# Kernel optimization log

Hardware: AMD Instinct MI355X
Metric: run time of the kernel (lower is better)

The kernel has to match this reference:

```python
import jax, jax.numpy as jnp
import numpy as np
import math

D = 512      # input_size == hidden_size
TAU = 4      # length of att/spatial lists
N = 16384    # tokens (batch*H*W)

def setup_inputs() -> dict:
    key = jax.random.key(0)
    ks = jax.random.split(key, 16)
    s = 1.0 / math.sqrt(D)
    return {
        "T_t": jax.random.normal(ks[0], (N, D), jnp.float32),
        "S_t": jax.random.normal(ks[1], (N, D), jnp.float32),
        "t_att": jax.random.normal(ks[2], (TAU, N, D), jnp.float32),
        "s_att": jax.random.normal(ks[3], (TAU, N, D), jnp.float32),
        "t_spatial": jax.random.normal(ks[4], (TAU, N, D), jnp.float32),
        "s_spatial": jax.random.normal(ks[5], (TAU, N, D), jnp.float32),
        # fl_t: Linear(D, 3D); fl_t_next: Linear(D, D); same for s
        "W_t": jax.random.uniform(ks[6], (3 * D, D), jnp.float32, -s, s),
        "b_t": jax.random.uniform(ks[7], (3 * D,), jnp.float32, -s, s),
        "W_tn": jax.random.uniform(ks[8], (D, D), jnp.float32, -s, s),
        "b_tn": jax.random.uniform(ks[9], (D,), jnp.float32, -s, s),
        "W_s": jax.random.uniform(ks[10], (3 * D, D), jnp.float32, -s, s),
        "b_s": jax.random.uniform(ks[11], (3 * D,), jnp.float32, -s, s),
        "W_sn": jax.random.uniform(ks[12], (D, D), jnp.float32, -s, s),
        "b_sn": jax.random.uniform(ks[13], (D,), jnp.float32, -s, s),
    }

def reference(T_t, S_t, t_att, s_att, t_spatial, s_spatial,
              W_t, b_t, W_tn, b_tn, W_s, b_s, W_sn, b_sn):
    d = T_t.shape[-1]
    scale = 1.0 / jnp.sqrt(jnp.asarray(d, T_t.dtype))
    s_next = S_t @ W_sn.T + b_sn          # [N, D]
    t_next = T_t @ W_tn.T + b_tn          # [N, D]

    # trend weights: dot-product along feature dim, softmax over tau axis
    w_s = jax.nn.softmax(jnp.einsum('knd,nd->kn', s_att, s_next) * scale, axis=0)
    w_t = jax.nn.softmax(jnp.einsum('knd,nd->kn', t_spatial, t_next) * scale, axis=0)
    T_trend = jnp.einsum('knd,kn->nd', t_att, w_s)      # [N, D]
    S_trend = jnp.einsum('knd,kn->nd', s_spatial, w_t)  # [N, D]

    t_gate = jax.nn.sigmoid(t_next)
    s_gate = jax.nn.sigmoid(s_next)
    T_fusion = T_t * t_gate + (1.0 - t_gate) * T_trend
    S_fusion = S_t * s_gate + (1.0 - s_gate) * S_trend

    T_concat = T_fusion @ W_t.T + b_t     # [N, 3D]
    S_concat = S_fusion @ W_s.T + b_s
    t_g, t_t, t_s = jnp.split(T_concat, 3, axis=1)
    s_g, s_t, s_s = jnp.split(S_concat, 3, axis=1)
    T_gate = jax.nn.sigmoid(t_g)
    S_gate = jax.nn.sigmoid(s_g)
    T_new = T_gate * t_t + (1.0 - T_gate) * s_t
    S_new = S_gate * s_s + (1.0 - S_gate) * t_s
    return T_new, S_new
```

## Files before the change

kernel.cpp:

```cpp
#include <hip/hip_runtime.h>

#define NTOK 16384
#define DIM 512
#define NTAU 4

typedef __attribute__((ext_vector_type(4))) float f32x4;
typedef __attribute__((ext_vector_type(8))) short bf16x8;
typedef __attribute__((ext_vector_type(4))) unsigned short u16x4;
typedef __attribute__((ext_vector_type(8))) unsigned short u16x8;

__device__ inline unsigned short f2bf(float f) {
    union { float f; unsigned int u; } v; v.f = f;
    unsigned int u = v.u + 0x7FFFu + ((v.u >> 16) & 1u);
    return (unsigned short)(u >> 16);
}

__global__ void convert_f32_bf16(const float* __restrict__ src,
                                 unsigned short* __restrict__ dst, int n4) {
    int i = blockIdx.x * blockDim.x + threadIdx.x;
    if (i < n4) {
        f32x4 v = ((const f32x4*)src)[i];
        u16x4 o;
        o[0] = f2bf(v[0]); o[1] = f2bf(v[1]); o[2] = f2bf(v[2]); o[3] = f2bf(v[3]);
        ((u16x4*)dst)[i] = o;
    }
}

__global__ __launch_bounds__(256, 2) void gemm_next(
    const float* __restrict__ A, const unsigned short* __restrict__ W,
    const float* __restrict__ bias, float* __restrict__ out)
{
    __shared__ unsigned short lA[128][40];
    __shared__ unsigned short lB[128][40];
    const int tid = threadIdx.x;
    const int m0 = blockIdx.y * 128;
    const int n0 = blockIdx.x * 128;
    const int lane = tid & 63;
    const int w = tid >> 6;
    const int wr = w >> 1, wc = w & 1;

    f32x4 acc[4][4];
#pragma unroll
    for (int i = 0; i < 4; i++)
#pragma unroll
        for (int j = 0; j < 4; j++) acc[i][j] = (f32x4){0.f, 0.f, 0.f, 0.f};

    const int arow = tid >> 3;
    const int acol = (tid & 7) * 4;
    const int brow = tid >> 2;
    const int bcol = (tid & 3) * 8;

    for (int k0 = 0; k0 < DIM; k0 += 32) {
#pragma unroll
        for (int i = 0; i < 4; i++) {
            int r = arow + 32 * i;
            f32x4 v = *(const f32x4*)(A + (size_t)(m0 + r) * DIM + k0 + acol);
            u16x4 o;
            o[0] = f2bf(v[0]); o[1] = f2bf(v[1]); o[2] = f2bf(v[2]); o[3] = f2bf(v[3]);
            *(u16x4*)&lA[r][acol] = o;
        }
#pragma unroll
        for (int i = 0; i < 2; i++) {
            int r = brow + 64 * i;
            u16x8 v = *(const u16x8*)(W + (size_t)(n0 + r) * DIM + k0 + bcol);
            *(u16x8*)&lB[r][bcol] = v;
        }
        __syncthreads();

        bf16x8 af[4], bfr[4];
#pragma unroll
        for (int i = 0; i < 4; i++)
            af[i] = *(const bf16x8*)&lA[wr * 64 + i * 16 + (lane & 15)][(lane >> 4) * 8];
#pragma unroll
        for (int j = 0; j < 4; j++)
            bfr[j] = *(const bf16x8*)&lB[wc * 64 + j * 16 + (lane & 15)][(lane >> 4) * 8];
#pragma unroll
        for (int i = 0; i < 4; i++)
#pragma unroll
            for (int j = 0; j < 4; j++)
                acc[i][j] = __builtin_amdgcn_mfma_f32_16x16x32_bf16(af[i], bfr[j], acc[i][j], 0, 0, 0);
        __syncthreads();
    }

#pragma unroll
    for (int j = 0; j < 4; j++) {
        int n = n0 + wc * 64 + j * 16 + (lane & 15);
        float bv = bias[n];
#pragma unroll
        for (int i = 0; i < 4; i++) {
            int mbase = m0 + wr * 64 + i * 16 + (lane >> 4) * 4;
#pragma unroll
            for (int r = 0; r < 4; r++)
                out[(size_t)(mbase + r) * DIM + n] = acc[i][j][r] + bv;
        }
    }
}

__global__ __launch_bounds__(256) void fuse_stream(
    const float* __restrict__ T_t, const float* __restrict__ S_t,
    const float* __restrict__ t_att, const float* __restrict__ s_att,
    const float* __restrict__ t_spatial, const float* __restrict__ s_spatial,
    const float* __restrict__ t_next, const float* __restrict__ s_next,
    unsigned short* __restrict__ Tf, unsigned short* __restrict__ Sf)
{
    const int lane = threadIdx.x & 63;
    const int wave = blockIdx.x * (blockDim.x >> 6) + (threadIdx.x >> 6);
    const int nwaves = gridDim.x * (blockDim.x >> 6);
    const float scale = 0.04419417382415922f;

    for (int n = wave; n < NTOK; n += nwaves) {
        const size_t rb = (size_t)n * DIM;
        const int c0 = lane * 4, c1 = 256 + lane * 4;
        f32x4 tn_a = *(const f32x4*)(t_next + rb + c0);
        f32x4 tn_b = *(const f32x4*)(t_next + rb + c1);
        f32x4 sn_a = *(const f32x4*)(s_next + rb + c0);
        f32x4 sn_b = *(const f32x4*)(s_next + rb + c1);

        float dws[NTAU], dwt[NTAU];
#pragma unroll
        for (int k = 0; k < NTAU; k++) {
            const size_t kb = ((size_t)k * NTOK + n) * DIM;
            f32x4 sa = *(const f32x4*)(s_att + kb + c0);
            f32x4 sb = *(const f32x4*)(s_att + kb + c1);
            f32x4 ta = *(const f32x4*)(t_spatial + kb + c0);
            f32x4 tb = *(const f32x4*)(t_spatial + kb + c1);
            dws[k] = sa[0]*sn_a[0]+sa[1]*sn_a[1]+sa[2]*sn_a[2]+sa[3]*sn_a[3]
                   + sb[0]*sn_b[0]+sb[1]*sn_b[1]+sb[2]*sn_b[2]+sb[3]*sn_b[3];
            dwt[k] = ta[0]*tn_a[0]+ta[1]*tn_a[1]+ta[2]*tn_a[2]+ta[3]*tn_a[3]
                   + tb[0]*tn_b[0]+tb[1]*tn_b[1]+tb[2]*tn_b[2]+tb[3]*tn_b[3];
        }
#pragma unroll
        for (int k = 0; k < NTAU; k++) {
            float v = dws[k];
#pragma unroll
            for (int off = 32; off; off >>= 1) v += __shfl_xor(v, off);
            dws[k] = v * scale;
            float u = dwt[k];
#pragma unroll
            for (int off = 32; off; off >>= 1) u += __shfl_xor(u, off);
            dwt[k] = u * scale;
        }
        float ms = fmaxf(fmaxf(dws[0], dws[1]), fmaxf(dws[2], dws[3]));
        float mt = fmaxf(fmaxf(dwt[0], dwt[1]), fmaxf(dwt[2], dwt[3]));
        float ws_[NTAU], wt_[NTAU], ssum = 0.f, tsum = 0.f;
#pragma unroll
        for (int k = 0; k < NTAU; k++) {
            ws_[k] = __expf(dws[k] - ms); ssum += ws_[k];
            wt_[k] = __expf(dwt[k] - mt); tsum += wt_[k];
        }
        float rs = 1.f / ssum, rt = 1.f / tsum;
#pragma unroll
        for (int k = 0; k < NTAU; k++) { ws_[k] *= rs; wt_[k] *= rt; }

        f32x4 Tta = {0,0,0,0}, Ttb = {0,0,0,0}, Sta = {0,0,0,0}, Stb = {0,0,0,0};
#pragma unroll
        for (int k = 0; k < NTAU; k++) {
            const size_t kb = ((size_t)k * NTOK + n) * DIM;
            f32x4 ta = *(const f32x4*)(t_att + kb + c0);
            f32x4 tb = *(const f32x4*)(t_att + kb + c1);
            f32x4 sa = *(const f32x4*)(s_spatial + kb + c0);
            f32x4 sb = *(const f32x4*)(s_spatial + kb + c1);
            float wk = ws_[k], vk = wt_[k];
#pragma unroll
            for (int e = 0; e < 4; e++) {
                Tta[e] += wk * ta[e]; Ttb[e] += wk * tb[e];
                Sta[e] += vk * sa[e]; Stb[e] += vk * sb[e];
            }
        }
        f32x4 Ta = *(const f32x4*)(T_t + rb + c0);
        f32x4 Tb = *(const f32x4*)(T_t + rb + c1);
        f32x4 Sa = *(const f32x4*)(S_t + rb + c0);
        f32x4 Sb = *(const f32x4*)(S_t + rb + c1);

        u16x4 oTa, oTb, oSa, oSb;
#pragma unroll
        for (int e = 0; e < 4; e++) {
            float gt_a = 1.f / (1.f + __expf(-tn_a[e]));
            float gt_b = 1.f / (1.f + __expf(-tn_b[e]));
            float gs_a = 1.f / (1.f + __expf(-sn_a[e]));
            float gs_b = 1.f / (1.f + __expf(-sn_b[e]));
            oTa[e] = f2bf(Ta[e] * gt_a + (1.f - gt_a) * Tta[e]);
            oTb[e] = f2bf(Tb[e] * gt_b + (1.f - gt_b) * Ttb[e]);
            oSa[e] = f2bf(Sa[e] * gs_a + (1.f - gs_a) * Sta[e]);
            oSb[e] = f2bf(Sb[e] * gs_b + (1.f - gs_b) * Stb[e]);
        }
        *(u16x4*)(Tf + rb + c0) = oTa;
        *(u16x4*)(Tf + rb + c1) = oTb;
        *(u16x4*)(Sf + rb + c0) = oSa;
        *(u16x4*)(Sf + rb + c1) = oSb;
    }
}

__global__ __launch_bounds__(256, 2) void gemm_final(
    const unsigned short* __restrict__ Tf, const unsigned short* __restrict__ Sf,
    const unsigned short* __restrict__ Wt, const unsigned short* __restrict__ Ws,
    const float* __restrict__ bt, const float* __restrict__ bs,
    float* __restrict__ out)
{
    __shared__ unsigned short lT[128][40];
    __shared__ unsigned short lS[128][40];
    __shared__ unsigned short lW[6][32][40];
    const int tid = threadIdx.x;
    const int m0 = blockIdx.y * 128;
    const int j0 = blockIdx.x * 32;
    const int lane = tid & 63;
    const int w = tid >> 6, wr = w >> 1, wc = w & 1;

    f32x4 acc[6][4];
#pragma unroll
    for (int g = 0; g < 6; g++)
#pragma unroll
        for (int i = 0; i < 4; i++) acc[g][i] = (f32x4){0.f, 0.f, 0.f, 0.f};

    const int arow = tid >> 2;
    const int acol = (tid & 3) * 8;

    for (int k0 = 0; k0 < DIM; k0 += 32) {
#pragma unroll
        for (int i = 0; i < 2; i++) {
            int r = arow + 64 * i;
            *(u16x8*)&lT[r][acol] = *(const u16x8*)(Tf + (size_t)(m0 + r) * DIM + k0 + acol);
            *(u16x8*)&lS[r][acol] = *(const u16x8*)(Sf + (size_t)(m0 + r) * DIM + k0 + acol);
        }
#pragma unroll
        for (int i = 0; i < 3; i++) {
            int c = tid + 256 * i;
            int g = c >> 7;
            int rr = (c >> 2) & 31;
            int ch = (c & 3) * 8;
            const unsigned short* src = (g < 3) ? Wt : Ws;
            int row = (g % 3) * DIM + j0 + rr;
            *(u16x8*)&lW[g][rr][ch] = *(const u16x8*)(src + (size_t)row * DIM + k0 + ch);
        }
        __syncthreads();

        bf16x8 aT[4], aS[4];
#pragma unroll
        for (int i = 0; i < 4; i++) {
            aT[i] = *(const bf16x8*)&lT[wr * 64 + i * 16 + (lane & 15)][(lane >> 4) * 8];
            aS[i] = *(const bf16x8*)&lS[wr * 64 + i * 16 + (lane & 15)][(lane >> 4) * 8];
        }
#pragma unroll
        for (int g = 0; g < 6; g++) {
            bf16x8 bw = *(const bf16x8*)&lW[g][wc * 16 + (lane & 15)][(lane >> 4) * 8];
#pragma unroll
            for (int i = 0; i < 4; i++)
                acc[g][i] = __builtin_amdgcn_mfma_f32_16x16x32_bf16(
                    (g < 3) ? aT[i] : aS[i], bw, acc[g][i], 0, 0, 0);
        }
        __syncthreads();
    }

    const int j = j0 + wc * 16 + (lane & 15);
    const float btg = bt[j], btt = bt[512 + j], bts = bt[1024 + j];
    const float bsg = bs[j], bst = bs[512 + j], bss = bs[1024 + j];
#pragma unroll
    for (int i = 0; i < 4; i++) {
        int mbase = m0 + wr * 64 + i * 16 + (lane >> 4) * 4;
#pragma unroll
        for (int r = 0; r < 4; r++) {
            float TG = acc[0][i][r] + btg;
            float TT = acc[1][i][r] + btt;
            float TS = acc[2][i][r] + bts;
            float SG = acc[3][i][r] + bsg;
            float ST = acc[4][i][r] + bst;
            float SS = acc[5][i][r] + bss;
            float gT = 1.f / (1.f + __expf(-TG));
            float gS = 1.f / (1.f + __expf(-SG));
            size_t m = (size_t)(mbase + r);
            out[m * DIM + j] = gT * TT + (1.f - gT) * ST;
            out[(size_t)NTOK * DIM + m * DIM + j] = gS * SS + (1.f - gS) * TS;
        }
    }
}

extern "C" void kernel_launch(void* const* d_in, const int* in_sizes, int n_in,
                              void* d_out, int out_size, void* d_ws, size_t ws_size,
                              hipStream_t stream) {
    const float* T_t       = (const float*)d_in[0];
    const float* S_t       = (const float*)d_in[1];
    const float* t_att     = (const float*)d_in[2];
    const float* s_att     = (const float*)d_in[3];
    const float* t_spatial = (const float*)d_in[4];
    const float* s_spatial = (const float*)d_in[5];
    const float* W_t  = (const float*)d_in[6];
    const float* b_t  = (const float*)d_in[7];
    const float* W_tn = (const float*)d_in[8];
    const float* b_tn = (const float*)d_in[9];
    const float* W_s  = (const float*)d_in[10];
    const float* b_s  = (const float*)d_in[11];
    const float* W_sn = (const float*)d_in[12];
    const float* b_sn = (const float*)d_in[13];
    float* out = (float*)d_out;

    char* ws = (char*)d_ws;
    float*          t_next = (float*)(ws + 0);
    float*          s_next = (float*)(ws + 33554432);
    unsigned short* Tf     = (unsigned short*)(ws + 67108864);
    unsigned short* Sf     = (unsigned short*)(ws + 83886080);
    unsigned short* Wtn_b  = (unsigned short*)(ws + 100663296);
    unsigned short* Wsn_b  = (unsigned short*)(ws + 101187584);
    unsigned short* Wt_b   = (unsigned short*)(ws + 101711872);
    unsigned short* Ws_b   = (unsigned short*)(ws + 103284736);

    const int n_sq = 512 * 512 / 4, n_big = 1536 * 512 / 4;
    convert_f32_bf16<<<(n_sq + 255) / 256, 256, 0, stream>>>(W_tn, Wtn_b, n_sq);
    convert_f32_bf16<<<(n_sq + 255) / 256, 256, 0, stream>>>(W_sn, Wsn_b, n_sq);
    convert_f32_bf16<<<(n_big + 255) / 256, 256, 0, stream>>>(W_t, Wt_b, n_big);
    convert_f32_bf16<<<(n_big + 255) / 256, 256, 0, stream>>>(W_s, Ws_b, n_big);

    dim3 g1(DIM / 128, NTOK / 128);
    gemm_next<<<g1, 256, 0, stream>>>(T_t, Wtn_b, b_tn, t_next);
    gemm_next<<<g1, 256, 0, stream>>>(S_t, Wsn_b, b_sn, s_next);

    fuse_stream<<<2048, 256, 0, stream>>>(T_t, S_t, t_att, s_att, t_spatial, s_spatial,
                                          t_next, s_next, Tf, Sf);

    dim3 g3(DIM / 32, NTOK / 128);
    gemm_final<<<g3, 256, 0, stream>>>(Tf, Sf, Wt_b, Ws_b, b_t, b_s, out);
}
```

Baseline: 303.0 us.

## Store next-projections as bf16 and process two tokens per wave with nontemporal loads

The t_next/s_next intermediates are now written by gemm_next as bf16 instead of fp32, which halves their write and read traffic between kernels. fuse_stream drops the grid-stride loop: each wave handles two tokens, each lane covers 8 contiguous features, and the streamed att/spatial tensors are read with nontemporal loads. The goal is less memory traffic and more loads in flight in this bandwidth-bound stage. The cost is lower precision in the gate and softmax-logit inputs, which now pass through bf16.

Result: no change. 305.8 us (+0.9%).

```diff
diff --git a/kernel.cpp b/kernel.cpp
--- a/kernel.cpp
+++ b/kernel.cpp
@@ -14,6 +14,16 @@
     unsigned int u = v.u + 0x7FFFu + ((v.u >> 16) & 1u);
     return (unsigned short)(u >> 16);
 }
+
+__device__ inline void bf8_to_f32(u16x8 h, f32x4& a, f32x4& b) {
+    union { unsigned int u; float f; } t;
+#pragma unroll
+    for (int e = 0; e < 4; e++) { t.u = ((unsigned int)h[e]) << 16; a[e] = t.f; }
+#pragma unroll
+    for (int e = 0; e < 4; e++) { t.u = ((unsigned int)h[4 + e]) << 16; b[e] = t.f; }
+}
+
+#define NTLOAD4(p) __builtin_nontemporal_load((const f32x4*)(p))
 
 __global__ void convert_f32_bf16(const float* __restrict__ src,
                                  unsigned short* __restrict__ dst, int n4) {
@@ -28,7 +38,7 @@
 
 __global__ __launch_bounds__(256, 2) void gemm_next(
     const float* __restrict__ A, const unsigned short* __restrict__ W,
-    const float* __restrict__ bias, float* __restrict__ out)
+    const float* __restrict__ bias, unsigned short* __restrict__ out)
 {
     __shared__ unsigned short lA[128][40];
     __shared__ unsigned short lB[128][40];
@@ -91,7 +101,7 @@
             int mbase = m0 + wr * 64 + i * 16 + (lane >> 4) * 4;
 #pragma unroll
             for (int r = 0; r < 4; r++)
-                out[(size_t)(mbase + r) * DIM + n] = acc[i][j][r] + bv;
+                out[(size_t)(mbase + r) * DIM + n] = f2bf(acc[i][j][r] + bv);
         }
     }
 }
@@ -100,94 +110,106 @@
     const float* __restrict__ T_t, const float* __restrict__ S_t,
     const float* __restrict__ t_att, const float* __restrict__ s_att,
     const float* __restrict__ t_spatial, const float* __restrict__ s_spatial,
-    const float* __restrict__ t_next, const float* __restrict__ s_next,
+    const unsigned short* __restrict__ t_next, const unsigned short* __restrict__ s_next,
     unsigned short* __restrict__ Tf, unsigned short* __restrict__ Sf)
 {
     const int lane = threadIdx.x & 63;
-    const int wave = blockIdx.x * (blockDim.x >> 6) + (threadIdx.x >> 6);
-    const int nwaves = gridDim.x * (blockDim.x >> 6);
+    const int w = blockIdx.x * 4 + (threadIdx.x >> 6);
     const float scale = 0.04419417382415922f;
-
-    for (int n = wave; n < NTOK; n += nwaves) {
-        const size_t rb = (size_t)n * DIM;
-        const int c0 = lane * 4, c1 = 256 + lane * 4;
-        f32x4 tn_a = *(const f32x4*)(t_next + rb + c0);
-        f32x4 tn_b = *(const f32x4*)(t_next + rb + c1);
-        f32x4 sn_a = *(const f32x4*)(s_next + rb + c0);
-        f32x4 sn_b = *(const f32x4*)(s_next + rb + c1);
-
-        float dws[NTAU], dwt[NTAU];
+    const int c = lane * 8;
+
+    const int n[2] = { 2 * w, 2 * w + 1 };
+    f32x4 tn_a[2], tn_b[2], sn_a[2], sn_b[2];
+#pragma unroll
+    for (int t = 0; t < 2; t++) {
+        const size_t rb = (size_t)n[t] * DIM + c;
+        bf8_to_f32(*(const u16x8*)(t_next + rb), tn_a[t], tn_b[t]);
+        bf8_to_f32(*(const u16x8*)(s_next + rb), sn_a[t], sn_b[t]);
+    }
+
+    float dws[2][NTAU], dwt[2][NTAU];
+#pragma unroll
+    for (int t = 0; t < 2; t++) {
 #pragma unroll
         for (int k = 0; k < NTAU; k++) {
-            const size_t kb = ((size_t)k * NTOK + n) * DIM;
-            f32x4 sa = *(const f32x4*)(s_att + kb + c0);
-            f32x4 sb = *(const f32x4*)(s_att + kb + c1);
-            f32x4 ta = *(const f32x4*)(t_spatial + kb + c0);
-            f32x4 tb = *(const f32x4*)(t_spatial + kb + c1);
-            dws[k] = sa[0]*sn_a[0]+sa[1]*sn_a[1]+sa[2]*sn_a[2]+sa[3]*sn_a[3]
-                   + sb[0]*sn_b[0]+sb[1]*sn_b[1]+sb[2]*sn_b[2]+sb[3]*sn_b[3];
-            dwt[k] = ta[0]*tn_a[0]+ta[1]*tn_a[1]+ta[2]*tn_a[2]+ta[3]*tn_a[3]
-                   + tb[0]*tn_b[0]+tb[1]*tn_b[1]+tb[2]*tn_b[2]+tb[3]*tn_b[3];
-        }
+            const size_t kb = ((size_t)k * NTOK + n[t]) * DIM + c;
+            f32x4 sa = NTLOAD4(s_att + kb);
+            f32x4 sb = NTLOAD4(s_att + kb + 4);
+            f32x4 ta = NTLOAD4(t_spatial + kb);
+            f32x4 tb = NTLOAD4(t_spatial + kb + 4);
+            dws[t][k] = sa[0]*sn_a[t][0]+sa[1]*sn_a[t][1]+sa[2]*sn_a[t][2]+sa[3]*sn_a[t][3]
+                      + sb[0]*sn_b[t][0]+sb[1]*sn_b[t][1]+sb[2]*sn_b[t][2]+sb[3]*sn_b[t][3];
+            dwt[t][k] = ta[0]*tn_a[t][0]+ta[1]*tn_a[t][1]+ta[2]*tn_a[t][2]+ta[3]*tn_a[t][3]
+                      + tb[0]*tn_b[t][0]+tb[1]*tn_b[t][1]+tb[2]*tn_b[t][2]+tb[3]*tn_b[t][3];
+        }
+    }
+#pragma unroll
+    for (int t = 0; t < 2; t++)
 #pragma unroll
         for (int k = 0; k < NTAU; k++) {
-            float v = dws[k];
+            float v = dws[t][k];
 #pragma unroll
             for (int off = 32; off; off >>= 1) v += __shfl_xor(v, off);
-            dws[k] = v * scale;
-            float u = dwt[k];
+            dws[t][k] = v * scale;
+            float u = dwt[t][k];
 #pragma unroll
             for (int off = 32; off; off >>= 1) u += __shfl_xor(u, off);
-            dwt[k] = u * scale;
-        }
-        float ms = fmaxf(fmaxf(dws[0], dws[1]), fmaxf(dws[2], dws[3]));
-        float mt = fmaxf(fmaxf(dwt[0], dwt[1]), fmaxf(dwt[2], dwt[3]));
-        float ws_[NTAU], wt_[NTAU], ssum = 0.f, tsum = 0.f;
+            dwt[t][k] = u * scale;
+        }
+
+    float ws_[2][NTAU], wt_[2][NTAU];
+#pragma unroll
+    for (int t = 0; t < 2; t++) {
+        float ms = fmaxf(fmaxf(dws[t][0], dws[t][1]), fmaxf(dws[t][2], dws[t][3]));
+        float mt = fmaxf(fmaxf(dwt[t][0], dwt[t][1]), fmaxf(dwt[t][2], dwt[t][3]));
+        float ssum = 0.f, tsum = 0.f;
 #pragma unroll
         for (int k = 0; k < NTAU; k++) {
-            ws_[k] = __expf(dws[k] - ms); ssum += ws_[k];
-            wt_[k] = __expf(dwt[k] - mt); tsum += wt_[k];
+            ws_[t][k] = __expf(dws[t][k] - ms); ssum += ws_[t][k];
+            wt_[t][k] = __expf(dwt[t][k] - mt); tsum += wt_[t][k];
         }
         float rs = 1.f / ssum, rt = 1.f / tsum;
 #pragma unroll
-        for (int k = 0; k < NTAU; k++) { ws_[k] *= rs; wt_[k] *= rt; }
-
+        for (int k = 0; k < NTAU; k++) { ws_[t][k] *= rs; wt_[t][k] *= rt; }
+    }
+
+#pragma unroll
+    for (int t = 0; t < 2; t++) {
+        const size_t rb = (size_t)n[t] * DIM + c;
         f32x4 Tta = {0,0,0,0}, Ttb = {0,0,0,0}, Sta = {0,0,0,0}, Stb = {0,0,0,0};
 #pragma unroll
         for (int k = 0; k < NTAU; k++) {
-            const size_t kb = ((size_t)k * NTOK + n) * DIM;
-            f32x4 ta = *(const f32x4*)(t_att + kb + c0);
-            f32x4 tb = *(const f32x4*)(t_att + kb + c1);
-            f32x4 sa = *(const f32x4*)(s_spatial + kb + c0);
-            f32x4 sb = *(const f32x4*)(s_spatial + kb + c1);
-            float wk = ws_[k], vk = wt_[k];
+            const size_t kb = ((size_t)k * NTOK + n[t]) * DIM + c;
+            f32x4 ta = NTLOAD4(t_att + kb);
+            f32x4 tb = NTLOAD4(t_att + kb + 4);
+            f32x4 sa = NTLOAD4(s_spatial + kb);
+            f32x4 sb = NTLOAD4(s_spatial + kb + 4);
+            float wk = ws_[t][k], vk = wt_[t][k];
 #pragma unroll
             for (int e = 0; e < 4; e++) {
                 Tta[e] += wk * ta[e]; Ttb[e] += wk * tb[e];
                 Sta[e] += vk * sa[e]; Stb[e] += vk * sb[e];
             }
         }
-        f32x4 Ta = *(const f32x4*)(T_t + rb + c0);
-        f32x4 Tb = *(const f32x4*)(T_t + rb + c1);
-        f32x4 Sa = *(const f32x4*)(S_t + rb + c0);
-        f32x4 Sb = *(const f32x4*)(S_t + rb + c1);
-
-        u16x4 oTa, oTb, oSa, oSb;
+        f32x4 Ta = *(const f32x4*)(T_t + rb);
+        f32x4 Tb = *(const f32x4*)(T_t + rb + 4);
+        f32x4 Sa = *(const f32x4*)(S_t + rb);
+        f32x4 Sb = *(const f32x4*)(S_t + rb + 4);
+
+        u16x8 oT, oS;
 #pragma unroll
         for (int e = 0; e < 4; e++) {
-            float gt_a = 1.f / (1.f + __expf(-tn_a[e]));
-            float gt_b = 1.f / (1.f + __expf(-tn_b[e]));
-            float gs_a = 1.f / (1.f + __expf(-sn_a[e]));
-            float gs_b = 1.f / (1.f + __expf(-sn_b[e]));
-            oTa[e] = f2bf(Ta[e] * gt_a + (1.f - gt_a) * Tta[e]);
-            oTb[e] = f2bf(Tb[e] * gt_b + (1.f - gt_b) * Ttb[e]);
-            oSa[e] = f2bf(Sa[e] * gs_a + (1.f - gs_a) * Sta[e]);
-            oSb[e] = f2bf(Sb[e] * gs_b + (1.f - gs_b) * Stb[e]);
-        }
-        *(u16x4*)(Tf + rb + c0) = oTa;
-        *(u16x4*)(Tf + rb + c1) = oTb;
-        *(u16x4*)(Sf + rb + c0) = oSa;
-        *(u16x4*)(Sf + rb + c1) = oSb;
+            float gt_a = 1.f / (1.f + __expf(-tn_a[t][e]));
+            float gt_b = 1.f / (1.f + __expf(-tn_b[t][e]));
+            float gs_a = 1.f / (1.f + __expf(-sn_a[t][e]));
+            float gs_b = 1.f / (1.f + __expf(-sn_b[t][e]));
+            oT[e]     = f2bf(Ta[e] * gt_a + (1.f - gt_a) * Tta[e]);
+            oT[4 + e] = f2bf(Tb[e] * gt_b + (1.f - gt_b) * Ttb[e]);
+            oS[e]     = f2bf(Sa[e] * gs_a + (1.f - gs_a) * Sta[e]);
+            oS[4 + e] = f2bf(Sb[e] * gs_b + (1.f - gs_b) * Stb[e]);
+        }
+        *(u16x8*)(Tf + rb) = oT;
+        *(u16x8*)(Sf + rb) = oS;
     }
 }
 
@@ -224,10 +246,10 @@
         }
 #pragma unroll
         for (int i = 0; i < 3; i++) {
-            int c = tid + 256 * i;
-            int g = c >> 7;
-            int rr = (c >> 2) & 31;
-            int ch = (c & 3) * 8;
+            int cidx = tid + 256 * i;
+            int g = cidx >> 7;
+            int rr = (cidx >> 2) & 31;
+            int ch = (cidx & 3) * 8;
             const unsigned short* src = (g < 3) ? Wt : Ws;
             int row = (g % 3) * DIM + j0 + rr;
             *(u16x8*)&lW[g][rr][ch] = *(const u16x8*)(src + (size_t)row * DIM + k0 + ch);
@@ -294,14 +316,14 @@
     float* out = (float*)d_out;
 
     char* ws = (char*)d_ws;
-    float*          t_next = (float*)(ws + 0);
-    float*          s_next = (float*)(ws + 33554432);
-    unsigned short* Tf     = (unsigned short*)(ws + 67108864);
-    unsigned short* Sf     = (unsigned short*)(ws + 83886080);
-    unsigned short* Wtn_b  = (unsigned short*)(ws + 100663296);
-    unsigned short* Wsn_b  = (unsigned short*)(ws + 101187584);
-    unsigned short* Wt_b   = (unsigned short*)(ws + 101711872);
-    unsigned short* Ws_b   = (unsigned short*)(ws + 103284736);
+    unsigned short* t_next = (unsigned short*)(ws + 0);
+    unsigned short* s_next = (unsigned short*)(ws + 16777216);
+    unsigned short* Tf     = (unsigned short*)(ws + 33554432);
+    unsigned short* Sf     = (unsigned short*)(ws + 50331648);
+    unsigned short* Wtn_b  = (unsigned short*)(ws + 67108864);
+    unsigned short* Wsn_b  = (unsigned short*)(ws + 67633152);
+    unsigned short* Wt_b   = (unsigned short*)(ws + 68157440);
+    unsigned short* Ws_b   = (unsigned short*)(ws + 69730304);
 
     const int n_sq = 512 * 512 / 4, n_big = 1536 * 512 / 4;
     convert_f32_bf16<<<(n_sq + 255) / 256, 256, 0, stream>>>(W_tn, Wtn_b, n_sq);
```
